# Performance work log

Measured on AMD Instinct MI355X. Metric: run time of the kernel, lower is better.

Reference implementation:

```python
import jax, jax.numpy as jnp
import numpy as np

EPS = 1e-5
B, N, K = 8, 4096, 20
C_FEAT = 64            # feature channels (C_in)
HEADS, DIM_K, DIM_V = 8, 32, 16   # C_out=128 -> dim_v = 128//8
CH = 64                # ch_raise
C_CAT = 2 * C_FEAT + DIM_V        # 144, concat channel dim
C_OUT = HEADS * DIM_V


def setup_inputs() -> dict:
    key = jax.random.key(0)
    ks = jax.random.split(key, 8)
    s = lambda k, shape: jax.random.normal(k, shape, jnp.float32) * 0.05
    return {
        "x": jax.random.normal(ks[0], (B, N, 3 + C_FEAT), jnp.float32),
        "W1": s(ks[1], (CH, C_CAT)), "g1": jnp.ones(CH), "b1": jnp.zeros(CH),
        "W2": s(ks[2], (CH, CH)),    "g2": jnp.ones(CH), "b2": jnp.zeros(CH),
        "Wv": s(ks[3], (DIM_V, C_CAT)), "gv": jnp.ones(DIM_V), "bv": jnp.zeros(DIM_V),
        "Wk": s(ks[4], (DIM_K, C_CAT)),
        "Wq": s(ks[5], (HEADS * DIM_K, CH)), "gq": jnp.ones(HEADS * DIM_K), "bq": jnp.zeros(HEADS * DIM_K),
        "Wh": s(ks[6], (DIM_V, 3)),
    }


def _bn(t, g, b):
    # BatchNorm (train-mode batch stats, biased var) over all axes but channel (last)
    axes = tuple(range(t.ndim - 1))
    mu = t.mean(axes, keepdims=True)
    var = t.var(axes, keepdims=True)
    return (t - mu) * jax.lax.rsqrt(var + EPS) * g + b


def reference(x, W1, g1, b1, W2, g2, b2, Wv, gv, bv, Wk, Wq, gq, bq, Wh):
    xyz = x[..., :3]                         # [B,N,3]
    feat = x[..., 3:]                        # [B,N,C_FEAT]
    # KNN via squared distances (same formula as square_distance)
    sq = jnp.sum(xyz * xyz, -1)              # [B,N]
    d = sq[:, :, None] + sq[:, None, :] - 2.0 * jnp.einsum('bnc,bmc->bnm', xyz, xyz)
    _, idx = jax.lax.top_k(-d, K)            # smallest K -> [B,N,K]
    bi = jnp.arange(B)[:, None, None]
    nb_xyz = xyz[bi, idx]                    # [B,N,K,3]
    nb_feat = feat[bi, idx]                  # [B,N,K,C_FEAT]
    gpn = nb_feat - feat[:, :, None, :]      # grouped_points_norm
    rel = nb_xyz - xyz[:, :, None, :]        # relative positions
    pos = jnp.einsum('vc,bnkc->bnkv', Wh, rel)   # mlp_h (1x1 conv)
    fcat = jnp.concatenate(
        [gpn, jnp.broadcast_to(feat[:, :, None, :], (B, N, K, C_FEAT)), pos], -1)  # [B,N,K,C_CAT]
    # mlp: two 1x1 conv + BN + ReLU, then max over K
    h = jax.nn.relu(_bn(jnp.einsum('oc,bnkc->bnko', W1, fcat), g1, b1))
    h = jax.nn.relu(_bn(jnp.einsum('oc,bnkc->bnko', W2, h), g2, b2))
    fq = h.max(2)                            # [B,N,CH]
    q = jax.nn.relu(_bn(jnp.einsum('oc,bnc->bno', Wq, fq), gq, bq))   # [B,N,H*DK]
    q = q.reshape(B, N, HEADS, DIM_K).transpose(0, 2, 3, 1)           # b h d n
    v = _bn(jnp.einsum('vc,bnkc->bnkv', Wv, fcat), gv, bv)            # [B,N,K,DIM_V]
    kk = jax.nn.softmax(jnp.einsum('dc,bnkc->bnkd', Wk, fcat), axis=2)  # softmax over K
    kv = jnp.einsum('bnkd,bnkv->bdvn', kk, v)                         # [B,DK,DV,N]
    out = jnp.einsum('bhdn,bdvn->bhvn', q, kv)                        # [B,H,DV,N]
    out = out.reshape(B, C_OUT, N)                                    # b (h v) n
    return (xyz, out)
```

## Files before the change

### kernel.cpp

```cpp
#include <hip/hip_runtime.h>
#include <hip/hip_bf16.h>

#define NB 8
#define NN 4096
#define KK 20
#define CFEAT 64
#define CCAT 144
#define CHN 64
#define NHEAD 8
#define DKK 32
#define DVV 16
#define NQC 256
#define EPSV 1e-5f
#define BNTOT (NB*NN)
#define ITEMS (BNTOT*KK)

typedef unsigned short ushort_t;
typedef __attribute__((ext_vector_type(8))) short bf16x8;
typedef __attribute__((ext_vector_type(4))) float f32x4;


__device__ __forceinline__ float wred(float v) {
#pragma unroll
  for (int off = 32; off > 0; off >>= 1) v += __shfl_down(v, off);
  return v;
}

__device__ __forceinline__ ushort_t f2bf(float f) {
  unsigned u = __float_as_uint(f);
  return (ushort_t)((u + 0x7fffu + ((u >> 16) & 1u)) >> 16);
}
__device__ __forceinline__ float bf2f(ushort_t h) {
  return __uint_as_float(((unsigned)h) << 16);
}

__device__ __forceinline__ float pdist(float4 me, float4 p) {
  float dot = fmaf(me.x, p.x, fmaf(me.y, p.y, me.z * p.z));
  return fmaf(-2.f, dot, me.w + p.w);
}

__device__ __forceinline__ void build_chunk(int ch,
    const float* __restrict__ fme, const float* __restrict__ fnb,
    float rx, float ry, float rz, const float* __restrict__ Wh, float* fc)
{
  if (ch < 4) {
    int c0 = ch * 16;
#pragma unroll
    for (int j = 0; j < 16; j += 4) {
      float4 a = *(const float4*)(fnb + c0 + j);
      float4 m = *(const float4*)(fme + c0 + j);
      fc[j + 0] = a.x - m.x; fc[j + 1] = a.y - m.y;
      fc[j + 2] = a.z - m.z; fc[j + 3] = a.w - m.w;
    }
  } else if (ch < 8) {
    int c0 = (ch - 4) * 16;
#pragma unroll
    for (int j = 0; j < 16; j += 4) {
      float4 m = *(const float4*)(fme + c0 + j);
      fc[j + 0] = m.x; fc[j + 1] = m.y; fc[j + 2] = m.z; fc[j + 3] = m.w;
    }
  } else {
#pragma unroll
    for (int v = 0; v < 16; ++v)
      fc[v] = fmaf(Wh[v * 3], rx, fmaf(Wh[v * 3 + 1], ry, Wh[v * 3 + 2] * rz));
  }
}

template<int NO>
__device__ __forceinline__ void accum_chunk(const float* __restrict__ W, int ch,
                                            const float* fc, float* acc)
{
  const float* wb = W + ch * 16;
#pragma unroll
  for (int o = 0; o < NO; ++o) {
    const float* w = wb + o * CCAT;
#pragma unroll
    for (int j = 0; j < 16; ++j) acc[o] = fmaf(w[j], fc[j], acc[o]);
  }
}


__global__ void __launch_bounds__(256) k_prep(const float* __restrict__ x,
                                              float4* __restrict__ xyz4,
                                              float* __restrict__ feat,
                                              float* __restrict__ outp)
{
  __shared__ float lx[256 * 67];
  int t = threadIdx.x;
  size_t base = (size_t)blockIdx.x * 256;
  const float* xb = x + base * 67;
#pragma unroll 4
  for (int j = t; j < 256 * 67; j += 256) lx[j] = xb[j];
  __syncthreads();
  {
    float a = lx[t * 67], b = lx[t * 67 + 1], c = lx[t * 67 + 2];
    xyz4[base + t] = make_float4(a, b, c, a * a + b * b + c * c);
  }
#pragma unroll
  for (int r = 0; r < 3; ++r) {
    int j = r * 256 + t;
    outp[base * 3 + j] = lx[(j / 3) * 67 + (j % 3)];
  }
#pragma unroll 8
  for (int j = t; j < 256 * 64; j += 256)
    feat[base * 64 + j] = lx[(j >> 6) * 67 + 3 + (j & 63)];
}

#define KNQ 64
#define KNS 8
__global__ void __launch_bounds__(512) k_knn(const float4* __restrict__ xyz4,
                                             int* __restrict__ idxb)
{
  __shared__ float sbd[KNS][KNQ][21];
  __shared__ float stau[KNQ];
  __shared__ int   scnt[KNQ];
  __shared__ int   stcnt[KNQ];
  __shared__ int   sties[KNQ * 16];
  int t = threadIdx.x;
  int q = t & 63, s = t >> 6;
  int b = blockIdx.x >> 6;
  int n = ((blockIdx.x & 63) << 6) + q;
  const float4* pts = xyz4 + (size_t)b * NN;
  float4 me = pts[n];
  if (t < KNQ) { scnt[t] = 0; stcnt[t] = 0; }
  int m0 = s << 9;
  float bd[KK];
#pragma unroll
  for (int j = 0; j < KK; ++j) bd[j] = 3.4e38f;
  float4 pc0 = pts[m0], pc1 = pts[m0 + 1], pc2 = pts[m0 + 2], pc3 = pts[m0 + 3];
#pragma unroll 1
  for (int m = m0; m < m0 + 512; m += 4) {
    float4 pn0 = pts[m + 4], pn1 = pts[m + 5], pn2 = pts[m + 6], pn3 = pts[m + 7];
    float d0 = pdist(me, pc0);
    float d1 = pdist(me, pc1);
    float d2 = pdist(me, pc2);
    float d3 = pdist(me, pc3);
#pragma unroll
    for (int j = KK - 1; j >= 1; --j)
      bd[j] = __builtin_amdgcn_fmed3f(d0, bd[j - 1], bd[j]);
    bd[0] = fminf(bd[0], d0);
#pragma unroll
    for (int j = KK - 1; j >= 1; --j)
      bd[j] = __builtin_amdgcn_fmed3f(d1, bd[j - 1], bd[j]);
    bd[0] = fminf(bd[0], d1);
#pragma unroll
    for (int j = KK - 1; j >= 1; --j)
      bd[j] = __builtin_amdgcn_fmed3f(d2, bd[j - 1], bd[j]);
    bd[0] = fminf(bd[0], d2);
#pragma unroll
    for (int j = KK - 1; j >= 1; --j)
      bd[j] = __builtin_amdgcn_fmed3f(d3, bd[j - 1], bd[j]);
    bd[0] = fminf(bd[0], d3);
    pc0 = pn0; pc1 = pn1; pc2 = pn2; pc3 = pn3;
  }
#pragma unroll
  for (int j = 0; j < KK; ++j) sbd[s][q][j] = bd[j];
  sbd[s][q][KK] = 3.4e38f;
  __syncthreads();
  if (t < KNQ) {
    int ia[KNS];
#pragma unroll
    for (int ss = 0; ss < KNS; ++ss) ia[ss] = 0;
    float tau = 0.f;
#pragma unroll 1
    for (int r = 0; r < KK; ++r) {
      float best = 3.5e38f; int bs = 0;
#pragma unroll
      for (int ss = 0; ss < KNS; ++ss) {
        float v = sbd[ss][t][ia[ss]];
        if (v < best) { best = v; bs = ss; }
      }
      ia[bs]++;
      tau = best;
    }
    stau[t] = tau;
  }
  __syncthreads();
  float tau = stau[q];
  size_t obase = ((size_t)b * NN + n) * KK;
#pragma unroll 2
  for (int m = m0; m < m0 + 512; ++m) {
    float4 p = pts[m];
    float d = pdist(me, p);
    if (d < tau) {
      int slot = atomicAdd(&scnt[q], 1);
      idxb[obase + slot] = m;
    } else if (d == tau) {
      int ts_ = atomicAdd(&stcnt[q], 1);
      if (ts_ < 16) sties[q * 16 + ts_] = m;
    }
  }
  __syncthreads();
  if (t < KNQ) {
    int c1 = scnt[t];
    int tc = min(stcnt[t], 16);
    int need = KK - c1;
    size_t ob = ((size_t)b * NN + (((blockIdx.x & 63) << 6) + t)) * KK;
    int last = -1;
#pragma unroll 1
    for (int r = 0; r < need; ++r) {
      int best = 0x7fffffff;
      for (int u = 0; u < tc; ++u) {
        int mv = sties[t * 16 + u];
        if (mv > last && mv < best) best = mv;
      }
      if (best == 0x7fffffff) best = 0;
      idxb[ob + c1 + r] = best;
      last = best;
    }
  }
}

__global__ void k_red1(const float* __restrict__ st1, const float* __restrict__ g1,
                       const float* __restrict__ b1, const float* __restrict__ gv,
                       const float* __restrict__ bv, float* __restrict__ par)
{
  int o = threadIdx.x;
  const float inv = 1.f / (float)ITEMS;
  if (o < 64) {
    float s = 0.f, s2 = 0.f;
    for (int j = 0; j < 64; ++j) { s += st1[j * 160 + o]; s2 += st1[j * 160 + 64 + o]; }
    float mu = s * inv, var = s2 * inv - mu * mu;
    float a = g1[o] * rsqrtf(var + EPSV);
    par[o] = a; par[64 + o] = b1[o] - mu * a;
  } else if (o < 80) {
    int v = o - 64;
    float s = 0.f, s2 = 0.f;
    for (int j = 0; j < 64; ++j) { s += st1[j * 160 + 128 + v]; s2 += st1[j * 160 + 144 + v]; }
    float mu = s * inv, var = s2 * inv - mu * mu;
    float a = gv[v] * rsqrtf(var + EPSV);
    par[128 + v] = a; par[144 + v] = bv[v] - mu * a;
  }
}

__global__ void k_red2(const float* __restrict__ st2, const float* __restrict__ g2,
                       const float* __restrict__ b2, float* __restrict__ par)
{
  int o = threadIdx.x;
  float s = 0.f, s2 = 0.f;
  for (int j = 0; j < 64; ++j) { s += st2[j * 128 + o]; s2 += st2[j * 128 + 64 + o]; }
  const float inv = 1.f / (float)ITEMS;
  float mu = s * inv, var = s2 * inv - mu * mu;
  float a = g2[o] * rsqrtf(var + EPSV);
  par[160 + o] = a; par[224 + o] = b2[o] - mu * a;
}


__global__ void __launch_bounds__(256, 2) k_g1(
    const float4* __restrict__ xyz4, const float* __restrict__ feat,
    const int* __restrict__ idxb, const float* __restrict__ W1,
    const float* __restrict__ Wv, const float* __restrict__ Wk,
    const float* __restrict__ Wh, float* __restrict__ st1,
    ushort_t* __restrict__ t1g, ushort_t* __restrict__ akg,
    ushort_t* __restrict__ tvg)
{
  __shared__ ushort_t lds[4][16][120];
  int tid = threadIdx.x;
  int w = tid >> 6, lane = tid & 63;
  int m = lane & 15, quad = lane >> 4;

  bf16x8 Bf[7][5];
#pragma unroll
  for (int nt = 0; nt < 7; ++nt) {
    const float* wrow = (nt < 4) ? (W1 + (nt * 16 + m) * CCAT)
                      : (nt == 4) ? (Wv + m * CCAT)
                      : (Wk + ((nt - 5) * 16 + m) * CCAT);
#pragma unroll
    for (int ks = 0; ks < 5; ++ks) {
      int c0 = ks * 32 + quad * 8;
      bf16x8 f;
      if (c0 < 144) {
        float4 u = *(const float4*)(wrow + c0);
        float4 v = *(const float4*)(wrow + c0 + 4);
        f[0] = (short)f2bf(u.x); f[1] = (short)f2bf(u.y);
        f[2] = (short)f2bf(u.z); f[3] = (short)f2bf(u.w);
        f[4] = (short)f2bf(v.x); f[5] = (short)f2bf(v.y);
        f[6] = (short)f2bf(v.z); f[7] = (short)f2bf(v.w);
      } else {
#pragma unroll
        for (int j = 0; j < 8; ++j) f[j] = 0;
      }
      Bf[nt][ks] = f;
    }
  }

  float ss[5], sq[5];
#pragma unroll
  for (int i = 0; i < 5; ++i) { ss[i] = 0.f; sq[i] = 0.f; }

#pragma unroll 1
  for (int t = 0; t < 4; ++t) {
    int tile = blockIdx.x * 16 + w * 4 + t;
    int item = tile * 16 + m;
    int bn = item / 20;
    int b = bn >> 12;
    int nb = idxb[item];
    const float* fme = feat + (size_t)bn * CFEAT;
    const float* fnb = feat + ((size_t)b * NN + nb) * CFEAT;
    float4 pm = xyz4[bn];
    float4 pn = xyz4[(size_t)b * NN + nb];
    float rx = pn.x - pm.x, ry = pn.y - pm.y, rz = pn.z - pm.z;

    f32x4 acc[7];
#pragma unroll
    for (int nt = 0; nt < 7; ++nt)
#pragma unroll
      for (int r = 0; r < 4; ++r) acc[nt][r] = 0.f;

#pragma unroll
    for (int ks = 0; ks < 5; ++ks) {
      int c0 = ks * 32 + quad * 8;
      bf16x8 A;
      if (c0 < 64) {
        float4 a0 = *(const float4*)(fnb + c0);
        float4 a1 = *(const float4*)(fnb + c0 + 4);
        float4 m0 = *(const float4*)(fme + c0);
        float4 m1 = *(const float4*)(fme + c0 + 4);
        A[0] = (short)f2bf(a0.x - m0.x); A[1] = (short)f2bf(a0.y - m0.y);
        A[2] = (short)f2bf(a0.z - m0.z); A[3] = (short)f2bf(a0.w - m0.w);
        A[4] = (short)f2bf(a1.x - m1.x); A[5] = (short)f2bf(a1.y - m1.y);
        A[6] = (short)f2bf(a1.z - m1.z); A[7] = (short)f2bf(a1.w - m1.w);
      } else if (c0 < 128) {
        int c = c0 - 64;
        float4 m0 = *(const float4*)(fme + c);
        float4 m1 = *(const float4*)(fme + c + 4);
        A[0] = (short)f2bf(m0.x); A[1] = (short)f2bf(m0.y);
        A[2] = (short)f2bf(m0.z); A[3] = (short)f2bf(m0.w);
        A[4] = (short)f2bf(m1.x); A[5] = (short)f2bf(m1.y);
        A[6] = (short)f2bf(m1.z); A[7] = (short)f2bf(m1.w);
      } else if (c0 < 144) {
        int v0 = c0 - 128;
#pragma unroll
        for (int j = 0; j < 8; ++j) {
          float pv = fmaf(Wh[(v0 + j) * 3], rx,
                     fmaf(Wh[(v0 + j) * 3 + 1], ry, Wh[(v0 + j) * 3 + 2] * rz));
          A[j] = (short)f2bf(pv);
        }
      } else {
#pragma unroll
        for (int j = 0; j < 8; ++j) A[j] = 0;
      }
#pragma unroll
      for (int nt = 0; nt < 7; ++nt)
        acc[nt] = __builtin_amdgcn_mfma_f32_16x16x32_bf16(A, Bf[nt][ks], acc[nt], 0, 0, 0);
    }

#pragma unroll
    for (int nt = 0; nt < 5; ++nt)
#pragma unroll
      for (int r = 0; r < 4; ++r) {
        float v = acc[nt][r];
        ss[nt] += v; sq[nt] += v * v;
      }

#pragma unroll
    for (int nt = 0; nt < 7; ++nt)
#pragma unroll
      for (int r = 0; r < 4; ++r)
        lds[w][quad * 4 + r][nt * 16 + m] = f2bf(acc[nt][r]);
    __syncthreads();

    {
      int it = lane >> 2, sg = lane & 3;
      const uint4* sp = (const uint4*)&lds[w][it][sg * 16];
      uint4 d0 = sp[0], d1 = sp[1];
      *(uint4*)(t1g + (size_t)tile * 1024 + lane * 16) = d0;
      *(uint4*)(t1g + (size_t)tile * 1024 + lane * 16 + 8) = d1;
      const uint4* spk = (const uint4*)&lds[w][it][80 + sg * 8];
      *(uint4*)(akg + (size_t)tile * 512 + lane * 8) = spk[0];
      if (lane < 32) {
        const uint4* spv = (const uint4*)&lds[w][lane >> 1][64 + (lane & 1) * 8];
        *(uint4*)(tvg + (size_t)tile * 256 + lane * 8) = spv[0];
      }
    }
    __syncthreads();
  }

  float* slot = st1 + (blockIdx.x & 63) * 160;
#pragma unroll
  for (int nt = 0; nt < 5; ++nt) {
    float s = ss[nt];
    s += __shfl_xor(s, 16); s += __shfl_xor(s, 32);
    float q = sq[nt];
    q += __shfl_xor(q, 16); q += __shfl_xor(q, 32);
    if (lane < 16) {
      if (nt < 4) {
        atomicAdd(&slot[nt * 16 + lane], s);
        atomicAdd(&slot[64 + nt * 16 + lane], q);
      } else {
        atomicAdd(&slot[128 + lane], s);
        atomicAdd(&slot[144 + lane], q);
      }
    }
  }
}

__global__ void __launch_bounds__(256) k_g2(
    const ushort_t* __restrict__ t1g, const float* __restrict__ W2,
    const float* __restrict__ par, float* __restrict__ st2,
    float* __restrict__ fqpre)
{
  __shared__ ushort_t lds[4][80][68];
  int tid = threadIdx.x;
  int w = tid >> 6, lane = tid & 63;
  int m = lane & 15, quad = lane >> 4;
  int gw = blockIdx.x * 4 + w;

  bf16x8 Bf[4][2];
#pragma unroll
  for (int nt = 0; nt < 4; ++nt) {
    const float* wrow = W2 + (nt * 16 + m) * CHN;
#pragma unroll
    for (int ks = 0; ks < 2; ++ks) {
      int c0 = ks * 32 + quad * 8;
      float4 u = *(const float4*)(wrow + c0);
      float4 v = *(const float4*)(wrow + c0 + 4);
      bf16x8 f;
      f[0] = (short)f2bf(u.x); f[1] = (short)f2bf(u.y);
      f[2] = (short)f2bf(u.z); f[3] = (short)f2bf(u.w);
      f[4] = (short)f2bf(v.x); f[5] = (short)f2bf(v.y);
      f[6] = (short)f2bf(v.z); f[7] = (short)f2bf(v.w);
      Bf[nt][ks] = f;
    }
  }
  float pa[2][8], pb[2][8];
#pragma unroll
  for (int ks = 0; ks < 2; ++ks) {
    int c0 = ks * 32 + quad * 8;
    float4 a0 = *(const float4*)(par + c0);
    float4 a1 = *(const float4*)(par + c0 + 4);
    float4 b0 = *(const float4*)(par + 64 + c0);
    float4 b1 = *(const float4*)(par + 64 + c0 + 4);
    pa[ks][0] = a0.x; pa[ks][1] = a0.y; pa[ks][2] = a0.z; pa[ks][3] = a0.w;
    pa[ks][4] = a1.x; pa[ks][5] = a1.y; pa[ks][6] = a1.z; pa[ks][7] = a1.w;
    pb[ks][0] = b0.x; pb[ks][1] = b0.y; pb[ks][2] = b0.z; pb[ks][3] = b0.w;
    pb[ks][4] = b1.x; pb[ks][5] = b1.y; pb[ks][6] = b1.z; pb[ks][7] = b1.w;
  }

  float ss[4] = {0.f, 0.f, 0.f, 0.f}, sq[4] = {0.f, 0.f, 0.f, 0.f};

#pragma unroll 1
  for (int t5 = 0; t5 < 5; ++t5) {
    int tile = gw * 5 + t5;
    int item = tile * 16 + m;
    f32x4 acc[4];
#pragma unroll
    for (int nt = 0; nt < 4; ++nt)
#pragma unroll
      for (int r = 0; r < 4; ++r) acc[nt][r] = 0.f;
#pragma unroll
    for (int ks = 0; ks < 2; ++ks) {
      const ushort_t* tp = t1g + (size_t)item * 64 + ks * 32 + quad * 8;
      uint4 raw = *(const uint4*)tp;
      unsigned rw[4] = {raw.x, raw.y, raw.z, raw.w};
      bf16x8 A;
#pragma unroll
      for (int i = 0; i < 4; ++i) {
        float lo = bf2f((ushort_t)(rw[i] & 0xffffu));
        float hi = bf2f((ushort_t)(rw[i] >> 16));
        float h0 = fmaxf(fmaf(lo, pa[ks][2 * i], pb[ks][2 * i]), 0.f);
        float h1 = fmaxf(fmaf(hi, pa[ks][2 * i + 1], pb[ks][2 * i + 1]), 0.f);
        A[2 * i] = (short)f2bf(h0);
        A[2 * i + 1] = (short)f2bf(h1);
      }
#pragma unroll
      for (int nt = 0; nt < 4; ++nt)
        acc[nt] = __builtin_amdgcn_mfma_f32_16x16x32_bf16(A, Bf[nt][ks], acc[nt], 0, 0, 0);
    }
#pragma unroll
    for (int nt = 0; nt < 4; ++nt)
#pragma unroll
      for (int r = 0; r < 4; ++r) {
        float v = acc[nt][r];
        ss[nt] += v; sq[nt] += v * v;
        lds[w][t5 * 16 + quad * 4 + r][nt * 16 + m] = f2bf(v);
      }
  }
  __syncthreads();

  {
    int bnl = lane >> 4;
    int chb = (lane & 15) * 4;
    float mx0 = -3.4e38f, mx1 = -3.4e38f, mx2 = -3.4e38f, mx3 = -3.4e38f;
    float mn0 = 3.4e38f, mn1 = 3.4e38f, mn2 = 3.4e38f, mn3 = 3.4e38f;
#pragma unroll
    for (int j = 0; j < KK; ++j) {
      const uint2 rv = *(const uint2*)&lds[w][bnl * 20 + j][chb];
      float v0 = bf2f((ushort_t)(rv.x & 0xffffu));
      float v1 = bf2f((ushort_t)(rv.x >> 16));
      float v2 = bf2f((ushort_t)(rv.y & 0xffffu));
      float v3 = bf2f((ushort_t)(rv.y >> 16));
      mx0 = fmaxf(mx0, v0); mn0 = fminf(mn0, v0);
      mx1 = fmaxf(mx1, v1); mn1 = fminf(mn1, v1);
      mx2 = fmaxf(mx2, v2); mn2 = fminf(mn2, v2);
      mx3 = fmaxf(mx3, v3); mn3 = fminf(mn3, v3);
    }
    int bn = gw * 4 + bnl;
    *(float4*)(fqpre + (size_t)bn * 128 + chb) = make_float4(mx0, mx1, mx2, mx3);
    *(float4*)(fqpre + (size_t)bn * 128 + 64 + chb) = make_float4(mn0, mn1, mn2, mn3);
  }

  float* slot = st2 + (blockIdx.x & 63) * 128;
#pragma unroll
  for (int nt = 0; nt < 4; ++nt) {
    float s = ss[nt];
    s += __shfl_xor(s, 16); s += __shfl_xor(s, 32);
    float q = sq[nt];
    q += __shfl_xor(q, 16); q += __shfl_xor(q, 32);
    if (lane < 16) {
      atomicAdd(&slot[nt * 16 + lane], s);
      atomicAdd(&slot[64 + nt * 16 + lane], q);
    }
  }
}

#define P3P 16
__global__ void __launch_bounds__(320, 2) k_p3s(
    const ushort_t* __restrict__ akg, const ushort_t* __restrict__ tvg,
    const float* __restrict__ par, __hip_bfloat16* __restrict__ kvg)
{
  __shared__ float sl[P3P][KK][DKK + 1];
  __shared__ float sv[P3P][KK][DVV + 1];
  __shared__ float sm[P3P][DKK], ssi[P3P][DKK];
  int tid = threadIdx.x;
  int p = tid / KK, k = tid - p * KK;
  size_t item = (size_t)(blockIdx.x * P3P + p) * KK + k;
  const unsigned* ap = (const unsigned*)(akg + item * DKK);
#pragma unroll
  for (int i = 0; i < DKK / 2; ++i) {
    unsigned wv = ap[i];
    sl[p][k][2 * i]     = __uint_as_float(wv << 16);
    sl[p][k][2 * i + 1] = __uint_as_float(wv & 0xffff0000u);
  }
  const unsigned* vp = (const unsigned*)(tvg + item * DVV);
#pragma unroll
  for (int i = 0; i < DVV / 2; ++i) {
    unsigned wv = vp[i];
    float lo = __uint_as_float(wv << 16);
    float hi = __uint_as_float(wv & 0xffff0000u);
    sv[p][k][2 * i]     = fmaf(lo, par[128 + 2 * i],     par[144 + 2 * i]);
    sv[p][k][2 * i + 1] = fmaf(hi, par[128 + 2 * i + 1], par[144 + 2 * i + 1]);
  }
  __syncthreads();
  for (int pd = tid; pd < P3P * DKK; pd += 320) {
    int pp = pd >> 5, d = pd & 31;
    float m = -1e30f;
#pragma unroll
    for (int q = 0; q < KK; ++q) m = fmaxf(m, sl[pp][q][d]);
    float S = 0.f;
#pragma unroll
    for (int q = 0; q < KK; ++q) S += __expf(sl[pp][q][d] - m);
    sm[pp][d] = m; ssi[pp][d] = 1.f / S;
  }
  __syncthreads();
  for (int pd = tid; pd < P3P * DKK; pd += 320) {
    int pp = pd >> 5, d = pd & 31;
    float m = sm[pp][d], Si = ssi[pp][d];
    float a[DVV];
#pragma unroll
    for (int v = 0; v < DVV; ++v) a[v] = 0.f;
#pragma unroll
    for (int q = 0; q < KK; ++q) {
      float wgt = __expf(sl[pp][q][d] - m) * Si;
#pragma unroll
      for (int v = 0; v < DVV; ++v) a[v] = fmaf(wgt, sv[pp][q][v], a[v]);
    }
    __hip_bfloat162* dst = (__hip_bfloat162*)
        (kvg + ((size_t)(blockIdx.x * P3P + pp) * DKK + d) * DVV);
#pragma unroll
    for (int v = 0; v < DVV; v += 2) {
      float2 f2; f2.x = a[v]; f2.y = a[v + 1];
      dst[v >> 1] = __float22bfloat162_rn(f2);
    }
  }
}

__global__ void __launch_bounds__(256) k_gq(
    const float* __restrict__ fqpre, const float* __restrict__ Wq,
    const float* __restrict__ par, float* __restrict__ stq,
    float* __restrict__ q2g)
{
  int tid = threadIdx.x;
  int w = tid >> 6, lane = tid & 63;
  int m = lane & 15, quad = lane >> 4;
  int nt0 = (w & 1) * 8;
  int mt = blockIdx.x * 2 + (w >> 1);

  bf16x8 Bf[8][2];
#pragma unroll
  for (int nt = 0; nt < 8; ++nt) {
    const float* wrow = Wq + ((nt0 + nt) * 16 + m) * CHN;
#pragma unroll
    for (int ks = 0; ks < 2; ++ks) {
      int c0 = ks * 32 + quad * 8;
      float4 u = *(const float4*)(wrow + c0);
      float4 v = *(const float4*)(wrow + c0 + 4);
      bf16x8 f;
      f[0] = (short)f2bf(u.x); f[1] = (short)f2bf(u.y);
      f[2] = (short)f2bf(u.z); f[3] = (short)f2bf(u.w);
      f[4] = (short)f2bf(v.x); f[5] = (short)f2bf(v.y);
      f[6] = (short)f2bf(v.z); f[7] = (short)f2bf(v.w);
      Bf[nt][ks] = f;
    }
  }

  f32x4 acc[8];
#pragma unroll
  for (int nt = 0; nt < 8; ++nt)
#pragma unroll
    for (int r = 0; r < 4; ++r) acc[nt][r] = 0.f;

  int item = mt * 16 + m;
  const float* fp = fqpre + (size_t)item * 128;
#pragma unroll
  for (int ks = 0; ks < 2; ++ks) {
    int c0 = ks * 32 + quad * 8;
    float mxv[8], mnv[8], av[8], bv[8];
    *(float4*)&mxv[0] = *(const float4*)(fp + c0);
    *(float4*)&mxv[4] = *(const float4*)(fp + c0 + 4);
    *(float4*)&mnv[0] = *(const float4*)(fp + 64 + c0);
    *(float4*)&mnv[4] = *(const float4*)(fp + 64 + c0 + 4);
    *(float4*)&av[0] = *(const float4*)(par + 160 + c0);
    *(float4*)&av[4] = *(const float4*)(par + 160 + c0 + 4);
    *(float4*)&bv[0] = *(const float4*)(par + 224 + c0);
    *(float4*)&bv[4] = *(const float4*)(par + 224 + c0 + 4);
    bf16x8 A;
#pragma unroll
    for (int j = 0; j < 8; ++j) {
      float pick = (av[j] >= 0.f) ? mxv[j] : mnv[j];
      float fq = fmaxf(fmaf(av[j], pick, bv[j]), 0.f);
      A[j] = (short)f2bf(fq);
    }
#pragma unroll
    for (int nt = 0; nt < 8; ++nt)
      acc[nt] = __builtin_amdgcn_mfma_f32_16x16x32_bf16(A, Bf[nt][ks], acc[nt], 0, 0, 0);
  }

  float* slot = stq + (blockIdx.x & 63) * 512;
#pragma unroll
  for (int nt = 0; nt < 8; ++nt) {
    int o = (nt0 + nt) * 16 + m;
    float s = 0.f, q = 0.f;
#pragma unroll
    for (int r = 0; r < 4; ++r) {
      float v = acc[nt][r];
      q2g[(size_t)(mt * 16 + quad * 4 + r) * NQC + o] = v;
      s += v; q += v * v;
    }
    s += __shfl_xor(s, 16); s += __shfl_xor(s, 32);
    q += __shfl_xor(q, 16); q += __shfl_xor(q, 32);
    if (lane < 16) {
      atomicAdd(&slot[(nt0 + nt) * 16 + lane], s);
      atomicAdd(&slot[256 + (nt0 + nt) * 16 + lane], q);
    }
  }
}

__global__ void k_redq(const float* __restrict__ stq, const float* __restrict__ gq,
                       const float* __restrict__ bq, float* __restrict__ par)
{
  int o = threadIdx.x;
  float s = 0.f, s2 = 0.f;
  for (int j = 0; j < 64; ++j) { s += stq[j * 512 + o]; s2 += stq[j * 512 + 256 + o]; }
  const float inv = 1.f / (float)BNTOT;
  float mu = s * inv, var = s2 * inv - mu * mu;
  float a = gq[o] * rsqrtf(var + EPSV);
  par[288 + o] = a; par[544 + o] = bq[o] - mu * a;
}

__global__ void __launch_bounds__(256) k_p4(const float* __restrict__ q2g,
                                            const __hip_bfloat16* __restrict__ kvg,
                                            const float* __restrict__ par,
                                            float* __restrict__ outp)
{
  __shared__ float sq2[4][NQC];
  __shared__ float skv[4][DKK * DVV];
  int t = threadIdx.x & 63, sub = threadIdx.x >> 6;
  int v = blockIdx.x * 4 + sub;
  int b = v & 7, n = v >> 3;
  int bn = (b << 12) | n;
#pragma unroll
  for (int j = 0; j < 8; ++j)
    skv[sub][t + 64 * j] = __bfloat162float(kvg[(size_t)bn * 512 + t + 64 * j]);
#pragma unroll
  for (int j = 0; j < 4; ++j) {
    int o = t + 64 * j;
    float q = q2g[(size_t)bn * NQC + o];
    sq2[sub][o] = fmaxf(fmaf(q, par[288 + o], par[544 + o]), 0.f);
  }
  __syncthreads();
#pragma unroll
  for (int j = 0; j < 2; ++j) {
    int ch = t + 64 * j, h = ch >> 4, vv = ch & 15;
    float a = 0.f;
#pragma unroll
    for (int d = 0; d < DKK; ++d) a = fmaf(sq2[sub][h * DKK + d], skv[sub][d * DVV + vv], a);
    outp[(size_t)BNTOT * 3 + ((size_t)(b * 128 + ch)) * NN + n] = a;
  }
}


__global__ void __launch_bounds__(256, 3) k_s1f(
    const float4* __restrict__ xyz4, const float* __restrict__ feat,
    const int* __restrict__ idxb, const float* __restrict__ W1,
    const float* __restrict__ Wv, const float* __restrict__ Wh,
    float* __restrict__ st1,
    __hip_bfloat16* __restrict__ t1g, __hip_bfloat16* __restrict__ tvg)
{
  int t = blockIdx.x * 256 + threadIdx.x;
  int bn = t / KK, k = t - bn * KK, b = bn >> 12;
  int nb = idxb[(size_t)bn * KK + k];
  const float* fme = feat + (size_t)bn * CFEAT;
  const float* fnb = feat + ((size_t)b * NN + nb) * CFEAT;
  float4 pn = xyz4[(size_t)b * NN + nb];
  float4 pm = xyz4[bn];
  float rx = pn.x - pm.x, ry = pn.y - pm.y, rz = pn.z - pm.z;
  float a1[CHN], av[DVV];
#pragma unroll
  for (int o = 0; o < CHN; ++o) a1[o] = 0.f;
#pragma unroll
  for (int o = 0; o < DVV; ++o) av[o] = 0.f;
#pragma unroll 1
  for (int ch = 0; ch < 9; ++ch) {
    float fc[16];
    build_chunk(ch, fme, fnb, rx, ry, rz, Wh, fc);
    accum_chunk<CHN>(W1, ch, fc, a1);
    accum_chunk<DVV>(Wv, ch, fc, av);
  }
  __hip_bfloat162* t1p = (__hip_bfloat162*)(t1g + (size_t)t * CHN);
#pragma unroll
  for (int o = 0; o < CHN; o += 2) {
    float2 f2; f2.x = a1[o]; f2.y = a1[o + 1];
    t1p[o >> 1] = __float22bfloat162_rn(f2);
  }
  __hip_bfloat162* tvp = (__hip_bfloat162*)(tvg + (size_t)t * DVV);
#pragma unroll
  for (int o = 0; o < DVV; o += 2) {
    float2 f2; f2.x = av[o]; f2.y = av[o + 1];
    tvp[o >> 1] = __float22bfloat162_rn(f2);
  }
  float* slot = st1 + (blockIdx.x & 63) * 160;
  int lane = threadIdx.x & 63;
#pragma unroll
  for (int o = 0; o < CHN; ++o) {
    float s = wred(a1[o]), s2 = wred(a1[o] * a1[o]);
    if (lane == 0) { atomicAdd(&slot[o], s); atomicAdd(&slot[CHN + o], s2); }
  }
#pragma unroll
  for (int o = 0; o < DVV; ++o) {
    float s = wred(av[o]), s2 = wred(av[o] * av[o]);
    if (lane == 0) { atomicAdd(&slot[128 + o], s); atomicAdd(&slot[128 + DVV + o], s2); }
  }
}

__global__ void __launch_bounds__(256, 4) k_skf(
    const float4* __restrict__ xyz4, const float* __restrict__ feat,
    const int* __restrict__ idxb, const float* __restrict__ Wk,
    const float* __restrict__ Wh, __hip_bfloat16* __restrict__ akg)
{
  int t = blockIdx.x * 256 + threadIdx.x;
  int bn = t / KK, k = t - bn * KK, b = bn >> 12;
  int nb = idxb[(size_t)bn * KK + k];
  const float* fme = feat + (size_t)bn * CFEAT;
  const float* fnb = feat + ((size_t)b * NN + nb) * CFEAT;
  float4 pn = xyz4[(size_t)b * NN + nb];
  float4 pm = xyz4[bn];
  float rx = pn.x - pm.x, ry = pn.y - pm.y, rz = pn.z - pm.z;
  float ak[DKK];
#pragma unroll
  for (int o = 0; o < DKK; ++o) ak[o] = 0.f;
#pragma unroll 1
  for (int ch = 0; ch < 9; ++ch) {
    float fc[16];
    build_chunk(ch, fme, fnb, rx, ry, rz, Wh, fc);
    accum_chunk<DKK>(Wk, ch, fc, ak);
  }
  __hip_bfloat162* akp = (__hip_bfloat162*)(akg + (size_t)t * DKK);
#pragma unroll
  for (int o = 0; o < DKK; o += 2) {
    float2 f2; f2.x = ak[o]; f2.y = ak[o + 1];
    akp[o >> 1] = __float22bfloat162_rn(f2);
  }
}

__global__ void __launch_bounds__(256, 4) k_s2f(
    const __hip_bfloat16* __restrict__ t1g, const float* __restrict__ W2,
    const float* __restrict__ par, float* __restrict__ st2)
{
  int t = blockIdx.x * 256 + threadIdx.x;
  const unsigned* tp = (const unsigned*)(t1g + (size_t)t * CHN);
  float h1[CHN];
#pragma unroll
  for (int i = 0; i < CHN / 2; ++i) {
    unsigned w = tp[i];
    float lo = __uint_as_float(w << 16);
    float hi = __uint_as_float(w & 0xffff0000u);
    h1[2 * i]     = fmaxf(fmaf(lo, par[2 * i],     par[64 + 2 * i]),     0.f);
    h1[2 * i + 1] = fmaxf(fmaf(hi, par[2 * i + 1], par[64 + 2 * i + 1]), 0.f);
  }
  float* slot = st2 + (blockIdx.x & 63) * 128;
  int lane = threadIdx.x & 63;
#pragma unroll 1
  for (int o = 0; o < CHN; ++o) {
    const float* w = W2 + o * CHN;
    float c0 = 0.f, c1 = 0.f, c2 = 0.f, c3 = 0.f;
#pragma unroll
    for (int c = 0; c < CHN; c += 4) {
      c0 = fmaf(w[c + 0], h1[c + 0], c0); c1 = fmaf(w[c + 1], h1[c + 1], c1);
      c2 = fmaf(w[c + 2], h1[c + 2], c2); c3 = fmaf(w[c + 3], h1[c + 3], c3);
    }
    float v = (c0 + c1) + (c2 + c3);
    float s = wred(v), s2 = wred(v * v);
    if (lane == 0) { atomicAdd(&slot[o], s); atomicAdd(&slot[64 + o], s2); }
  }
}

__global__ void __launch_bounds__(320, 2) k_p3f(
    const __hip_bfloat16* __restrict__ t1g, const __hip_bfloat16* __restrict__ akg,
    const __hip_bfloat16* __restrict__ tvg, const float* __restrict__ W2,
    const float* __restrict__ par, float* __restrict__ fqg,
    __hip_bfloat16* __restrict__ kvg)
{
  __shared__ float sl[P3P][KK][DKK + 1];
  __shared__ float sv[P3P][KK][DVV + 1];
  __shared__ unsigned sfq[P3P][CHN];
  __shared__ float sm[P3P][DKK], ssi[P3P][DKK];
  int tid = threadIdx.x;
  for (int i = tid; i < P3P * CHN; i += 320) ((unsigned*)sfq)[i] = 0u;
  __syncthreads();
  int p = tid / KK, k = tid - p * KK;
  size_t item = (size_t)(blockIdx.x * P3P + p) * KK + k;
  const unsigned* ap = (const unsigned*)(akg + item * DKK);
#pragma unroll
  for (int i = 0; i < DKK / 2; ++i) {
    unsigned w = ap[i];
    sl[p][k][2 * i]     = __uint_as_float(w << 16);
    sl[p][k][2 * i + 1] = __uint_as_float(w & 0xffff0000u);
  }
  const unsigned* vp = (const unsigned*)(tvg + item * DVV);
#pragma unroll
  for (int i = 0; i < DVV / 2; ++i) {
    unsigned w = vp[i];
    float lo = __uint_as_float(w << 16);
    float hi = __uint_as_float(w & 0xffff0000u);
    sv[p][k][2 * i]     = fmaf(lo, par[128 + 2 * i],     par[144 + 2 * i]);
    sv[p][k][2 * i + 1] = fmaf(hi, par[128 + 2 * i + 1], par[144 + 2 * i + 1]);
  }
  const unsigned* tp = (const unsigned*)(t1g + item * CHN);
  float h1[CHN];
#pragma unroll
  for (int i = 0; i < CHN / 2; ++i) {
    unsigned w = tp[i];
    float lo = __uint_as_float(w << 16);
    float hi = __uint_as_float(w & 0xffff0000u);
    h1[2 * i]     = fmaxf(fmaf(lo, par[2 * i],     par[64 + 2 * i]),     0.f);
    h1[2 * i + 1] = fmaxf(fmaf(hi, par[2 * i + 1], par[64 + 2 * i + 1]), 0.f);
  }
#pragma unroll 1
  for (int o = 0; o < CHN; ++o) {
    const float* w = W2 + o * CHN;
    float c0 = 0.f, c1 = 0.f, c2 = 0.f, c3 = 0.f;
#pragma unroll
    for (int c = 0; c < CHN; c += 4) {
      c0 = fmaf(w[c + 0], h1[c + 0], c0); c1 = fmaf(w[c + 1], h1[c + 1], c1);
      c2 = fmaf(w[c + 2], h1[c + 2], c2); c3 = fmaf(w[c + 3], h1[c + 3], c3);
    }
    float v = (c0 + c1) + (c2 + c3);
    float h2 = fmaxf(fmaf(v, par[160 + o], par[224 + o]), 0.f);
    atomicMax(&sfq[p][o], __float_as_uint(h2));
  }
  __syncthreads();
  for (int i = tid; i < P3P * CHN; i += 320)
    fqg[(size_t)blockIdx.x * (P3P * CHN) + i] = __uint_as_float(sfq[i >> 6][i & 63]);
  for (int pd = tid; pd < P3P * DKK; pd += 320) {
    int pp = pd >> 5, d = pd & 31;
    float m = -1e30f;
#pragma unroll
    for (int q = 0; q < KK; ++q) m = fmaxf(m, sl[pp][q][d]);
    float S = 0.f;
#pragma unroll
    for (int q = 0; q < KK; ++q) S += __expf(sl[pp][q][d] - m);
    sm[pp][d] = m; ssi[pp][d] = 1.f / S;
  }
  __syncthreads();
  for (int pd = tid; pd < P3P * DKK; pd += 320) {
    int pp = pd >> 5, d = pd & 31;
    float m = sm[pp][d], Si = ssi[pp][d];
    float a[DVV];
#pragma unroll
    for (int v = 0; v < DVV; ++v) a[v] = 0.f;
#pragma unroll
    for (int q = 0; q < KK; ++q) {
      float wgt = __expf(sl[pp][q][d] - m) * Si;
#pragma unroll
      for (int v = 0; v < DVV; ++v) a[v] = fmaf(wgt, sv[pp][q][v], a[v]);
    }
    __hip_bfloat162* dst = (__hip_bfloat162*)
        (kvg + ((size_t)(blockIdx.x * P3P + pp) * DKK + d) * DVV);
#pragma unroll
    for (int v = 0; v < DVV; v += 2) {
      float2 f2; f2.x = a[v]; f2.y = a[v + 1];
      dst[v >> 1] = __float22bfloat162_rn(f2);
    }
  }
}

__global__ void __launch_bounds__(128, 2) k_pqf(const float* __restrict__ fqg,
                                                const float* __restrict__ Wq,
                                                float* __restrict__ stq,
                                                float* __restrict__ q2g)
{
  int bn = blockIdx.x * 128 + threadIdx.x;
  float fq[CHN];
#pragma unroll
  for (int c = 0; c < CHN; c += 4) {
    float4 v4 = *(const float4*)(fqg + (size_t)bn * CHN + c);
    fq[c] = v4.x; fq[c + 1] = v4.y; fq[c + 2] = v4.z; fq[c + 3] = v4.w;
  }
  float* slot = stq + (blockIdx.x & 63) * 512;
  int lane = threadIdx.x & 63;
#pragma unroll 1
  for (int o = 0; o < NQC; ++o) {
    const float* w = Wq + o * CHN;
    float a0 = 0.f, a1 = 0.f, a2 = 0.f, a3 = 0.f;
#pragma unroll
    for (int c = 0; c < CHN; c += 4) {
      a0 = fmaf(w[c], fq[c], a0); a1 = fmaf(w[c + 1], fq[c + 1], a1);
      a2 = fmaf(w[c + 2], fq[c + 2], a2); a3 = fmaf(w[c + 3], fq[c + 3], a3);
    }
    float v = (a0 + a1) + (a2 + a3);
    q2g[(size_t)bn * NQC + o] = v;
    float s = wred(v), s2 = wred(v * v);
    if (lane == 0) { atomicAdd(&slot[o], s); atomicAdd(&slot[256 + o], s2); }
  }
}

__global__ void __launch_bounds__(64) k_p4f(const float* __restrict__ q2g,
                                            const __hip_bfloat16* __restrict__ kvg,
                                            const float* __restrict__ par,
                                            float* __restrict__ outp)
{
  __shared__ float sq2[NQC], skv[DKK * DVV];
  int t = threadIdx.x;
  int b = blockIdx.x & 7, n = blockIdx.x >> 3;
  int bn = (b << 12) | n;
#pragma unroll
  for (int j = 0; j < 8; ++j)
    skv[t + 64 * j] = __bfloat162float(kvg[(size_t)bn * 512 + t + 64 * j]);
#pragma unroll
  for (int j = 0; j < 4; ++j) {
    int o = t + 64 * j;
    float v = q2g[(size_t)bn * NQC + o];
    sq2[o] = fmaxf(fmaf(v, par[288 + o], par[544 + o]), 0.f);
  }
  __syncthreads();
#pragma unroll
  for (int j = 0; j < 2; ++j) {
    int ch = t + 64 * j, h = ch >> 4, vv = ch & 15;
    float a = 0.f;
#pragma unroll
    for (int d = 0; d < DKK; ++d) a = fmaf(sq2[h * DKK + d], skv[d * DVV + vv], a);
    outp[(size_t)BNTOT * 3 + ((size_t)(b * 128 + ch)) * NN + n] = a;
  }
}


extern "C" void kernel_launch(void* const* d_in, const int* in_sizes, int n_in,
                              void* d_out, int out_size, void* d_ws, size_t ws_size,
                              hipStream_t stream)
{
  const float* x  = (const float*)d_in[0];
  const float* W1 = (const float*)d_in[1];
  const float* g1 = (const float*)d_in[2];
  const float* b1 = (const float*)d_in[3];
  const float* W2 = (const float*)d_in[4];
  const float* g2 = (const float*)d_in[5];
  const float* b2 = (const float*)d_in[6];
  const float* Wv = (const float*)d_in[7];
  const float* gv = (const float*)d_in[8];
  const float* bv = (const float*)d_in[9];
  const float* Wk = (const float*)d_in[10];
  const float* Wq = (const float*)d_in[11];
  const float* gq = (const float*)d_in[12];
  const float* bq = (const float*)d_in[13];
  const float* Wh = (const float*)d_in[14];

  float* ws = (float*)d_ws;
  float4* xyz4 = (float4*)ws;
  float*  feat = ws + 131072;
  int*    idxb = (int*)(ws + 2228224);
  float*  st1  = ws + 2883584;
  float*  st2  = ws + 2893824;
  float*  stq  = ws + 2902016;
  float*  par  = ws + 2934784;
  float*  fqg  = ws + 2935584;
  __hip_bfloat16* kvg = (__hip_bfloat16*)(ws + 5032736);
  float*  outp = (float*)d_out;

  ushort_t* t1g = (ushort_t*)(ws + 13421344);
  ushort_t* akg = (ushort_t*)(ws + 34392864);
  ushort_t* tvg = (ushort_t*)(ws + 44878624);
  float*    fqpre = ws + 50121504;
  float*    q2g = ws + 13421344;

  const size_t NEW_NEED  = (size_t)54315808 * 4;

  hipMemsetAsync(st1, 0, (size_t)(10240 + 8192 + 32768) * sizeof(float), stream);
  k_prep<<<128, 256, 0, stream>>>(x, xyz4, feat, outp);
  k_knn <<<512, 512, 0, stream>>>(xyz4, idxb);

  if (ws_size >= NEW_NEED) {
    k_g1  <<<2560, 256, 0, stream>>>(xyz4, feat, idxb, W1, Wv, Wk, Wh, st1, t1g, akg, tvg);
    k_red1<<<1, 128, 0, stream>>>(st1, g1, b1, gv, bv, par);
    k_g2  <<<2048, 256, 0, stream>>>(t1g, W2, par, st2, fqpre);
    k_red2<<<1, 64, 0, stream>>>(st2, g2, b2, par);
    k_p3s <<<2048, 320, 0, stream>>>(akg, tvg, par, kvg);
    k_gq  <<<1024, 256, 0, stream>>>(fqpre, Wq, par, stq, q2g);
    k_redq<<<1, 256, 0, stream>>>(stq, gq, bq, par);
    k_p4  <<<8192, 256, 0, stream>>>(q2g, kvg, par, outp);
  } else {
    __hip_bfloat16* t1b = (__hip_bfloat16*)t1g;
    __hip_bfloat16* akb = (__hip_bfloat16*)akg;
    __hip_bfloat16* tvb = (__hip_bfloat16*)tvg;
    float* q2f = ws + 34392864;
    k_s1f <<<2560, 256, 0, stream>>>(xyz4, feat, idxb, W1, Wv, Wh, st1, t1b, tvb);
    k_skf <<<2560, 256, 0, stream>>>(xyz4, feat, idxb, Wk, Wh, akb);
    k_red1<<<1, 128, 0, stream>>>(st1, g1, b1, gv, bv, par);
    k_s2f <<<2560, 256, 0, stream>>>(t1b, W2, par, st2);
    k_red2<<<1, 64, 0, stream>>>(st2, g2, b2, par);
    k_p3f <<<2048, 320, 0, stream>>>(t1b, akb, tvb, W2, par, fqg, kvg);
    k_pqf <<<256, 128, 0, stream>>>(fqg, Wq, stq, q2f);
    k_redq<<<1, 256, 0, stream>>>(stq, gq, bq, par);
    k_p4f <<<32768, 64, 0, stream>>>(q2f, kvg, par, outp);
  }
}
```

Baseline: 603.2 us.

## Split KNN scan across 12 waves and tile final q·kv output over 32 points

The KNN kernel now splits the candidate range over 12 slices per query group instead of 8, with uneven slice bounds and a scalar tail loop, raising occupancy and shortening each thread's serial insertion chain. The final output kernel is restructured so each block handles 32 consecutive points of one batch: q and packed bf16 kv are staged transposed in padded shared memory, and each thread keeps its head's 32 q values in registers. Output stores along n are now coalesced where the old version wrote with stride N per point. The cost is a larger merge step in KNN, more shared memory per block in both kernels, and more registers in the output kernel.

```diff
diff --git a/kernel.cpp b/kernel.cpp
--- a/kernel.cpp
+++ b/kernel.cpp
@@ -39,6 +39,13 @@
   return fmaf(-2.f, dot, me.w + p.w);
 }
 
+__device__ __forceinline__ void insert20(float* bd, float d) {
+#pragma unroll
+  for (int j = KK - 1; j >= 1; --j)
+    bd[j] = __builtin_amdgcn_fmed3f(d, bd[j - 1], bd[j]);
+  bd[0] = fminf(bd[0], d);
+}
+
 __device__ __forceinline__ void build_chunk(int ch,
     const float* __restrict__ fme, const float* __restrict__ fnb,
     float rx, float ry, float rz, const float* __restrict__ Wh, float* fc)
@@ -107,8 +114,8 @@
 }
 
 #define KNQ 64
-#define KNS 8
-__global__ void __launch_bounds__(512) k_knn(const float4* __restrict__ xyz4,
+#define KNS 12
+__global__ void __launch_bounds__(768) k_knn(const float4* __restrict__ xyz4,
                                              int* __restrict__ idxb)
 {
   __shared__ float sbd[KNS][KNQ][21];
@@ -123,35 +130,30 @@
   const float4* pts = xyz4 + (size_t)b * NN;
   float4 me = pts[n];
   if (t < KNQ) { scnt[t] = 0; stcnt[t] = 0; }
-  int m0 = s << 9;
+  int m_lo = (s * NN) / KNS;
+  int m_hi = ((s + 1) * NN) / KNS;
+  int m4e = m_lo + ((m_hi - m_lo) & ~3);
   float bd[KK];
 #pragma unroll
   for (int j = 0; j < KK; ++j) bd[j] = 3.4e38f;
-  float4 pc0 = pts[m0], pc1 = pts[m0 + 1], pc2 = pts[m0 + 2], pc3 = pts[m0 + 3];
+  float4 pc0 = pts[m_lo], pc1 = pts[m_lo + 1], pc2 = pts[m_lo + 2], pc3 = pts[m_lo + 3];
 #pragma unroll 1
-  for (int m = m0; m < m0 + 512; m += 4) {
+  for (int m = m_lo; m < m4e; m += 4) {
     float4 pn0 = pts[m + 4], pn1 = pts[m + 5], pn2 = pts[m + 6], pn3 = pts[m + 7];
     float d0 = pdist(me, pc0);
     float d1 = pdist(me, pc1);
     float d2 = pdist(me, pc2);
     float d3 = pdist(me, pc3);
-#pragma unroll
-    for (int j = KK - 1; j >= 1; --j)
-      bd[j] = __builtin_amdgcn_fmed3f(d0, bd[j - 1], bd[j]);
-    bd[0] = fminf(bd[0], d0);
-#pragma unroll
-    for (int j = KK - 1; j >= 1; --j)
-      bd[j] = __builtin_amdgcn_fmed3f(d1, bd[j - 1], bd[j]);
-    bd[0] = fminf(bd[0], d1);
-#pragma unroll
-    for (int j = KK - 1; j >= 1; --j)
-      bd[j] = __builtin_amdgcn_fmed3f(d2, bd[j - 1], bd[j]);
-    bd[0] = fminf(bd[0], d2);
-#pragma unroll
-    for (int j = KK - 1; j >= 1; --j)
-      bd[j] = __builtin_amdgcn_fmed3f(d3, bd[j - 1], bd[j]);
-    bd[0] = fminf(bd[0], d3);
+    insert20(bd, d0);
+    insert20(bd, d1);
+    insert20(bd, d2);
+    insert20(bd, d3);
     pc0 = pn0; pc1 = pn1; pc2 = pn2; pc3 = pn3;
+  }
+#pragma unroll 1
+  for (int m = m4e; m < m_hi; ++m) {
+    float d = pdist(me, pts[m]);
+    insert20(bd, d);
   }
 #pragma unroll
   for (int j = 0; j < KK; ++j) sbd[s][q][j] = bd[j];
@@ -179,7 +181,7 @@
   float tau = stau[q];
   size_t obase = ((size_t)b * NN + n) * KK;
 #pragma unroll 2
-  for (int m = m0; m < m0 + 512; ++m) {
+  for (int m = m_lo; m < m_hi; ++m) {
     float4 p = pts[m];
     float d = pdist(me, p);
     if (d < tau) {
@@ -673,29 +675,41 @@
                                             const float* __restrict__ par,
                                             float* __restrict__ outp)
 {
-  __shared__ float sq2[4][NQC];
-  __shared__ float skv[4][DKK * DVV];
-  int t = threadIdx.x & 63, sub = threadIdx.x >> 6;
-  int v = blockIdx.x * 4 + sub;
-  int b = v & 7, n = v >> 3;
-  int bn = (b << 12) | n;
-#pragma unroll
-  for (int j = 0; j < 8; ++j)
-    skv[sub][t + 64 * j] = __bfloat162float(kvg[(size_t)bn * 512 + t + 64 * j]);
-#pragma unroll
-  for (int j = 0; j < 4; ++j) {
-    int o = t + 64 * j;
-    float q = q2g[(size_t)bn * NQC + o];
-    sq2[sub][o] = fmaxf(fmaf(q, par[288 + o], par[544 + o]), 0.f);
-  }
-  __syncthreads();
-#pragma unroll
-  for (int j = 0; j < 2; ++j) {
-    int ch = t + 64 * j, h = ch >> 4, vv = ch & 15;
-    float a = 0.f;
-#pragma unroll
-    for (int d = 0; d < DKK; ++d) a = fmaf(sq2[sub][h * DKK + d], skv[sub][d * DVV + vv], a);
-    outp[(size_t)BNTOT * 3 + ((size_t)(b * 128 + ch)) * NN + n] = a;
+  __shared__ float sq2[NQC][33];
+  __shared__ unsigned skv[NQC][33];
+  int t = threadIdx.x;
+  int b = blockIdx.x >> 7, nc = blockIdx.x & 127;
+  int bn0 = (b << 12) | (nc << 5);
+#pragma unroll 4
+  for (int i = t; i < 32 * NQC; i += 256) {
+    int n = i >> 8, o = i & 255;
+    float q = q2g[(size_t)(bn0 + n) * NQC + o];
+    sq2[o][n] = fmaxf(fmaf(q, par[288 + o], par[544 + o]), 0.f);
+  }
+  const unsigned* kvp = (const unsigned*)kvg;
+#pragma unroll 4
+  for (int i = t; i < 32 * 256; i += 256) {
+    int n = i >> 8, dv2 = i & 255;
+    skv[dv2][n] = kvp[(size_t)(bn0 + n) * 256 + dv2];
+  }
+  __syncthreads();
+  int n = t & 31, h = t >> 5;
+  float qr[DKK];
+#pragma unroll
+  for (int d = 0; d < DKK; ++d) qr[d] = sq2[h * DKK + d][n];
+  int n_out = (nc << 5) + n;
+  size_t ob = (size_t)BNTOT * 3 + (size_t)(b * 128 + h * 16) * NN + n_out;
+#pragma unroll
+  for (int vv = 0; vv < DVV; vv += 2) {
+    float a0 = 0.f, a1 = 0.f;
+#pragma unroll
+    for (int d = 0; d < DKK; ++d) {
+      unsigned pk = skv[(d * DVV + vv) >> 1][n];
+      a0 = fmaf(qr[d], bf2f((ushort_t)(pk & 0xffffu)), a0);
+      a1 = fmaf(qr[d], bf2f((ushort_t)(pk >> 16)), a1);
+    }
+    outp[ob + (size_t)vv * NN] = a0;
+    outp[ob + (size_t)(vv + 1) * NN] = a1;
   }
 }
 
@@ -1007,7 +1021,7 @@
 
   hipMemsetAsync(st1, 0, (size_t)(10240 + 8192 + 32768) * sizeof(float), stream);
   k_prep<<<128, 256, 0, stream>>>(x, xyz4, feat, outp);
-  k_knn <<<512, 512, 0, stream>>>(xyz4, idxb);
+  k_knn <<<512, 768, 0, stream>>>(xyz4, idxb);
 
   if (ws_size >= NEW_NEED) {
     k_g1  <<<2560, 256, 0, stream>>>(xyz4, feat, idxb, W1, Wv, Wk, Wh, st1, t1g, akg, tvg);
@@ -1017,7 +1031,7 @@
     k_p3s <<<2048, 320, 0, stream>>>(akg, tvg, par, kvg);
     k_gq  <<<1024, 256, 0, stream>>>(fqpre, Wq, par, stq, q2g);
     k_redq<<<1, 256, 0, stream>>>(stq, gq, bq, par);
-    k_p4  <<<8192, 256, 0, stream>>>(q2g, kvg, par, outp);
+    k_p4  <<<1024, 256, 0, stream>>>(q2g, kvg, par, outp);
   } else {
     __hip_bfloat16* t1b = (__hip_bfloat16*)t1g;
     __hip_bfloat16* akb = (__hip_bfloat16*)akg;
```

New measurement: 573.6 us. 1.05x faster.
